# Kernel tuning notes

Measured on AMD Instinct MI355X. Metric: run time of the kernel, lower is better.

Reference implementation:

```python
import jax, jax.numpy as jnp
import numpy as np

EPS = 1e-6  # matches F.normalize / safe_div eps in vector-quantize-pytorch
IN_COMMIT_W = 0.25
COMMIT_W = 1.0


def _safe_div(num, den):
    return num / jnp.clip(den, EPS, None)


def _l2norm(t):
    n = jnp.linalg.norm(t, axis=-1, keepdims=True)
    return t / jnp.clip(n, EPS, None)


def setup_inputs() -> dict:
    key = jax.random.key(0)
    k1, k2, k3 = jax.random.split(key, 3)
    b, n, dim, c = 8, 1024, 512, 4096
    x = jax.random.normal(k1, (b, n, dim), jnp.float32)
    # frozen codebook init: randn * dim**-0.5 (as in __init__)
    frozen_codebook = jax.random.normal(k2, (c, dim), jnp.float32) * dim ** -0.5
    # nn.Linear(dim, dim, bias=False) weight, shape [out, in]
    weight = jax.random.normal(k3, (dim, dim), jnp.float32) * dim ** -0.5
    return {"x": x, "frozen_codebook": frozen_codebook, "weight": weight}


def simvq_forward(x, frozen_codebook, weight):
    # implicit codebook: frozen codes passed through linear transform -> [c, d]
    codebook = frozen_codebook @ weight.T

    # nearest-code search (torch.no_grad): squared distances have same argmin as cdist
    xs = jax.lax.stop_gradient(x)
    cs = jax.lax.stop_gradient(codebook)
    d2 = (jnp.sum(xs * xs, axis=-1, keepdims=True)
          - 2.0 * jnp.einsum('bnd,cd->bnc', xs, cs)
          + jnp.sum(cs * cs, axis=-1))  # [b, n, c]
    indices = jnp.argmin(d2, axis=-1)  # [b, n]

    quantized = codebook[indices]  # [b, n, d]

    # commitment loss: mse(x.detach(), q) + mse(x, q.detach()) * 0.25
    commit_loss = (jnp.mean((jax.lax.stop_gradient(x) - quantized) ** 2)
                   + IN_COMMIT_W * jnp.mean((x - jax.lax.stop_gradient(quantized)) ** 2))

    # rotation trick (Fifty et al.): rotate x onto quantized, grads flow as rotation
    nx = jnp.linalg.norm(x, axis=-1, keepdims=True)
    nq = jnp.linalg.norm(quantized, axis=-1, keepdims=True)
    u = _safe_div(x, nx)
    q = _safe_div(quantized, nq)
    w = jax.lax.stop_gradient(_l2norm(u + q))
    e = x
    ew = jnp.sum(e * w, axis=-1, keepdims=True)
    eu = jnp.sum(e * jax.lax.stop_gradient(u), axis=-1, keepdims=True)
    rotated = e - 2.0 * ew * w + 2.0 * eu * jax.lax.stop_gradient(q)
    rotated = rotated * jax.lax.stop_gradient(_safe_div(nq, nx))

    return rotated, indices, commit_loss * COMMIT_W


def reference(x, frozen_codebook, weight):
    return simvq_forward(x, frozen_codebook, weight)
```

## Files before the change

kernel.cpp:

```cpp
#include <hip/hip_runtime.h>
#include <hip/hip_bf16.h>
#include <cstdint>


#define R_ROWS 8192
#define DIM    512
#define NCODES 4096
#define BK     16
#define MARGIN      1.5e-2f
#define TILE_MARGIN 1.8e-2f

typedef __attribute__((ext_vector_type(8))) _Float16 f16x8;
typedef __attribute__((ext_vector_type(4))) float f32x4;
typedef __attribute__((ext_vector_type(8))) unsigned short ushort8;

__device__ __forceinline__ void gload_lds16(const void* g, void* l) {
    __builtin_amdgcn_global_load_lds(
        (const __attribute__((address_space(1))) void*)g,
        (__attribute__((address_space(3))) void*)l, 16, 0, 0);
}

template<int BM, int BN, int TM, int TN, bool ARGMIN>
__launch_bounds__(256)
__global__ void gemm_nt(const float* __restrict__ A, const float* __restrict__ Bm,
                        float* __restrict__ Cout,
                        const float* __restrict__ rowAdd, const float* __restrict__ colAdd,
                        float* __restrict__ pVal, int* __restrict__ pIdx,
                        int M, int N, int K) {
    constexpr int THREADS = (BM / TM) * (BN / TN);
    constexpr int PAD = 4;
    __shared__ float As[BK][BM + PAD];
    __shared__ float Bs[BK][BN + PAD];

    const int tid = threadIdx.x;
    const int tx = tid % (BN / TN);
    const int ty = tid / (BN / TN);
    const int rowBase = blockIdx.y * BM;
    const int colBase = blockIdx.x * BN;

    float acc[TM][TN];
#pragma unroll
    for (int i = 0; i < TM; i++)
#pragma unroll
        for (int j = 0; j < TN; j++) acc[i][j] = 0.f;

    constexpr int A_F4 = BM * BK / 4;
    constexpr int B_F4 = BN * BK / 4;
    const int nK = K / BK;

    for (int kt = 0; kt < nK; ++kt) {
        const int k0 = kt * BK;
#pragma unroll
        for (int f = 0; f < A_F4 / THREADS; ++f) {
            int e = tid + f * THREADS;
            int row = e >> 2;
            int kq = e & 3;
            float4 v = *reinterpret_cast<const float4*>(
                &A[(size_t)(rowBase + row) * K + k0 + kq * 4]);
            As[kq * 4 + 0][row] = v.x; As[kq * 4 + 1][row] = v.y;
            As[kq * 4 + 2][row] = v.z; As[kq * 4 + 3][row] = v.w;
        }
#pragma unroll
        for (int f = 0; f < B_F4 / THREADS; ++f) {
            int e = tid + f * THREADS;
            int row = e >> 2;
            int kq = e & 3;
            float4 v = *reinterpret_cast<const float4*>(
                &Bm[(size_t)(colBase + row) * K + k0 + kq * 4]);
            Bs[kq * 4 + 0][row] = v.x; Bs[kq * 4 + 1][row] = v.y;
            Bs[kq * 4 + 2][row] = v.z; Bs[kq * 4 + 3][row] = v.w;
        }
        __syncthreads();

#pragma unroll
        for (int k = 0; k < BK; k++) {
            float a[TM], b[TN];
#pragma unroll
            for (int i4 = 0; i4 < TM / 4; i4++) {
                float4 v = *reinterpret_cast<const float4*>(&As[k][ty * TM + i4 * 4]);
                a[i4 * 4 + 0] = v.x; a[i4 * 4 + 1] = v.y;
                a[i4 * 4 + 2] = v.z; a[i4 * 4 + 3] = v.w;
            }
#pragma unroll
            for (int j4 = 0; j4 < TN / 4; j4++) {
                float4 v = *reinterpret_cast<const float4*>(&Bs[k][tx * TN + j4 * 4]);
                b[j4 * 4 + 0] = v.x; b[j4 * 4 + 1] = v.y;
                b[j4 * 4 + 2] = v.z; b[j4 * 4 + 3] = v.w;
            }
#pragma unroll
            for (int i = 0; i < TM; i++)
#pragma unroll
                for (int j = 0; j < TN; j++) acc[i][j] = fmaf(a[i], b[j], acc[i][j]);
        }
        __syncthreads();
    }

    if constexpr (!ARGMIN) {
#pragma unroll
        for (int i = 0; i < TM; i++) {
#pragma unroll
            for (int j4 = 0; j4 < TN / 4; j4++) {
                float4 v = make_float4(acc[i][j4 * 4 + 0], acc[i][j4 * 4 + 1],
                                       acc[i][j4 * 4 + 2], acc[i][j4 * 4 + 3]);
                *reinterpret_cast<float4*>(
                    &Cout[(size_t)(rowBase + ty * TM + i) * N + colBase + tx * TN + j4 * 4]) = v;
            }
        }
    } else {
        constexpr int TX = BN / TN;
        __shared__ float rV[BM][TX + 1];
        __shared__ int   rI[BM][TX + 1];
        float xn[TM];
#pragma unroll
        for (int i = 0; i < TM; i++) xn[i] = rowAdd[rowBase + ty * TM + i];
        float cn[TN];
#pragma unroll
        for (int j = 0; j < TN; j++) cn[j] = colAdd[colBase + tx * TN + j];

#pragma unroll
        for (int i = 0; i < TM; i++) {
            float bv = 3.402823466e38f; int bi = 0;
#pragma unroll
            for (int j = 0; j < TN; j++) {
                float s = xn[i] + cn[j] - 2.f * acc[i][j];
                if (s < bv) { bv = s; bi = colBase + tx * TN + j; }
            }
            rV[ty * TM + i][tx] = bv;
            rI[ty * TM + i][tx] = bi;
        }
        __syncthreads();
        if (tid < BM) {
            float bv = 3.402823466e38f; int bi = 0;
#pragma unroll
            for (int t = 0; t < TX; t++) {
                float v = rV[tid][t];
                if (v < bv) { bv = v; bi = rI[tid][t]; }
            }
            int gr = rowBase + tid;
            pVal[(size_t)gr * gridDim.x + blockIdx.x] = bv;
            pIdx[(size_t)gr * gridDim.x + blockIdx.x] = bi;
        }
    }
}

__global__ void rowsumsq_cast(const float* __restrict__ src, float* __restrict__ dst,
                              ushort* __restrict__ h16, int nRows) {
    int gw = (blockIdx.x * blockDim.x + threadIdx.x) >> 6;
    int lane = threadIdx.x & 63;
    if (gw >= nRows) return;
    const float4* s4 = reinterpret_cast<const float4*>(src + (size_t)gw * DIM);
    float4 a = s4[lane];
    float4 b = s4[lane + 64];
    float s = a.x * a.x + a.y * a.y + a.z * a.z + a.w * a.w
            + b.x * b.x + b.y * b.y + b.z * b.z + b.w * b.w;

    ushort ha[4], hb[4];
    {
        _Float16 t0 = (_Float16)a.x, t1 = (_Float16)a.y,
                 t2 = (_Float16)a.z, t3 = (_Float16)a.w;
        ha[0] = *reinterpret_cast<unsigned short*>(&t0);
        ha[1] = *reinterpret_cast<unsigned short*>(&t1);
        ha[2] = *reinterpret_cast<unsigned short*>(&t2);
        ha[3] = *reinterpret_cast<unsigned short*>(&t3);
        _Float16 u0 = (_Float16)b.x, u1 = (_Float16)b.y,
                 u2 = (_Float16)b.z, u3 = (_Float16)b.w;
        hb[0] = *reinterpret_cast<unsigned short*>(&u0);
        hb[1] = *reinterpret_cast<unsigned short*>(&u1);
        hb[2] = *reinterpret_cast<unsigned short*>(&u2);
        hb[3] = *reinterpret_cast<unsigned short*>(&u3);
    }
    ushort* rowp = h16 + (size_t)gw * DIM;
    *reinterpret_cast<uint2*>(rowp + lane * 4)       = *reinterpret_cast<uint2*>(ha);
    *reinterpret_cast<uint2*>(rowp + 256 + lane * 4) = *reinterpret_cast<uint2*>(hb);

#pragma unroll
    for (int o = 32; o; o >>= 1) s += __shfl_xor(s, o);
    if (lane == 0) dst[gw] = s;
}

__global__ void rowsumsq(const float* __restrict__ src, float* __restrict__ dst, int nRows) {
    int gw = (blockIdx.x * blockDim.x + threadIdx.x) >> 6;
    int lane = threadIdx.x & 63;
    if (gw >= nRows) return;
    const float4* s4 = reinterpret_cast<const float4*>(src + (size_t)gw * DIM);
    float4 a = s4[lane];
    float4 b = s4[lane + 64];
    float s = a.x * a.x + a.y * a.y + a.z * a.z + a.w * a.w
            + b.x * b.x + b.y * b.y + b.z * b.z + b.w * b.w;
#pragma unroll
    for (int o = 32; o; o >>= 1) s += __shfl_xor(s, o);
    if (lane == 0) dst[gw] = s;
}

__device__ __forceinline__ f16x8 read_frag(const char* half_base, int row, int g) {
    int gp = g ^ ((row >> 1) & 3);
    return *reinterpret_cast<const f16x8*>(half_base + row * 64 + gp * 16);
}

__device__ __forceinline__ void stage128(const ushort* __restrict__ src, int rowBase,
                                         int segElem, char* ldsBase, int tid) {
#pragma unroll
    for (int i = 0; i < 2; ++i) {
        int o = i * 4096 + tid * 16;
        int row = o >> 6;
        int gp  = (o >> 4) & 3;
        int g   = gp ^ ((row >> 1) & 3);
        const char* gsrc = (const char*)src + (size_t)(rowBase + row) * 1024
                         + (size_t)segElem * 2 + g * 16;
        gload_lds16(gsrc, ldsBase + i * 4096 + (tid >> 6) * 1024);
    }
}

__launch_bounds__(256)
__global__ void score_mfma4(const ushort* __restrict__ xh, const ushort* __restrict__ ch,
                            const float* __restrict__ xn2, const float* __restrict__ cn2,
                            float* __restrict__ pV1, float* __restrict__ pV2,
                            int* __restrict__ pI1) {
    __shared__ __align__(16) ushort As[4096];
    __shared__ __align__(16) ushort Bs[4096];

    int bid = blockIdx.x;
    int swz = (bid & 7) * 256 + (bid >> 3);
    int tileN = swz & 31;
    int tileM = swz >> 5;
    int rowBase = tileM * 128, colBase = tileN * 128;

    int tid = threadIdx.x, lane = tid & 63, w = tid >> 6;
    int wr = w >> 1, wc = w & 1;
    int g = lane >> 4, c15 = lane & 15;

    f32x4 acc[4][4];
#pragma unroll
    for (int m = 0; m < 4; m++)
#pragma unroll
        for (int n = 0; n < 4; n++) acc[m][n] = (f32x4){0.f, 0.f, 0.f, 0.f};

    for (int kk = 0; kk < 16; ++kk) {
        int se = kk * 32;
        stage128(xh, rowBase, se, (char*)As, tid);
        stage128(ch, colBase, se, (char*)Bs, tid);
        __syncthreads();

        f16x8 af[4], bf[4];
#pragma unroll
        for (int m = 0; m < 4; ++m)
            af[m] = read_frag((const char*)As, wr * 64 + m * 16 + c15, g);
#pragma unroll
        for (int n = 0; n < 4; ++n)
            bf[n] = read_frag((const char*)Bs, wc * 64 + n * 16 + c15, g);
#pragma unroll
        for (int m = 0; m < 4; ++m)
#pragma unroll
            for (int n = 0; n < 4; ++n)
                acc[m][n] = __builtin_amdgcn_mfma_f32_16x16x32_f16(
                    af[m], bf[n], acc[m][n], 0, 0, 0);
        __syncthreads();
    }

    float cnv[4];
#pragma unroll
    for (int n = 0; n < 4; ++n) cnv[n] = cn2[colBase + wc * 64 + n * 16 + c15];

    size_t gbase = (size_t)(tileN * 2 + wc) * R_ROWS + rowBase;
#pragma unroll
    for (int m = 0; m < 4; ++m) {
#pragma unroll
        for (int j = 0; j < 4; ++j) {
            int rl = wr * 64 + m * 16 + g * 4 + j;
            float xn = xn2[rowBase + rl];
            float v1 = 3.402823466e38f, v2 = 3.402823466e38f; int i1 = 0x7fffffff;
#pragma unroll
            for (int n = 0; n < 4; ++n) {
                float s = xn + cnv[n] - 2.f * acc[m][n][j];
                int ci = colBase + wc * 64 + n * 16 + c15;
                if (s < v1 || (s == v1 && ci < i1)) { v2 = v1; v1 = s; i1 = ci; }
                else if (s < v2) v2 = s;
            }
#pragma unroll
            for (int off = 1; off < 16; off <<= 1) {
                float ov1 = __shfl_xor(v1, off);
                int   oi1 = __shfl_xor(i1, off);
                float ov2 = __shfl_xor(v2, off);
                if (ov1 < v1 || (ov1 == v1 && oi1 < i1)) {
                    v2 = fminf(v1, ov2); v1 = ov1; i1 = oi1;
                } else {
                    v2 = fminf(v2, ov1);
                }
            }
            if (c15 == 0) {
                size_t o = gbase + rl;
                pV1[o] = v1; pV2[o] = v2; pI1[o] = i1;
            }
        }
    }
}

__global__ void combine_flag(const float* __restrict__ pV1, const float* __restrict__ pV2,
                             const int* __restrict__ pI1,
                             int* __restrict__ idx, float* __restrict__ idxF,
                             int* __restrict__ flag, float* __restrict__ vminOut) {
    int r = blockIdx.x * blockDim.x + threadIdx.x;
    if (r >= R_ROWS) return;
    float v1 = 3.402823466e38f, v2 = 3.402823466e38f; int i1 = 0x7fffffff;
    for (int t = 0; t < 64; ++t) {
        float a1 = pV1[(size_t)t * R_ROWS + r];
        float a2 = pV2[(size_t)t * R_ROWS + r];
        int   ai = pI1[(size_t)t * R_ROWS + r];
        if (a1 < v1 || (a1 == v1 && ai < i1)) { v2 = fminf(v1, a2); v1 = a1; i1 = ai; }
        else { v2 = fminf(v2, a1); }
    }
    idx[r] = i1;
    idxF[r] = (float)i1;
    vminOut[r] = v1;
    flag[r] = (v2 - v1 < MARGIN) ? 1 : 0;
}

__launch_bounds__(256)
__global__ void refine_rows(const float* __restrict__ x, const float* __restrict__ cb,
                            const float* __restrict__ xn2, const float* __restrict__ cn2,
                            const float* __restrict__ pV1, const float* __restrict__ vmin,
                            const int* __restrict__ flag,
                            int* __restrict__ idx, float* __restrict__ idxF) {
    int r = blockIdx.x;
    if (flag[r] == 0) return;

    __shared__ float xs[DIM];
    __shared__ float wv[4];
    __shared__ int   wi[4];
    __shared__ unsigned long long maskS;
    int tid = threadIdx.x, lane = tid & 63, w = tid >> 6;

    for (int i = tid; i < DIM; i += 256) xs[i] = x[(size_t)r * DIM + i];

    float thr = vmin[r] + TILE_MARGIN;
    if (tid < 64) {
        float gm = pV1[(size_t)tid * R_ROWS + r];
        unsigned long long b = __ballot(gm <= thr);
        if (tid == 0) maskS = b;
    }
    __syncthreads();

    float x0 = xs[lane * 4 + 0], x1 = xs[lane * 4 + 1];
    float x2 = xs[lane * 4 + 2], x3 = xs[lane * 4 + 3];
    float y0 = xs[256 + lane * 4 + 0], y1 = xs[256 + lane * 4 + 1];
    float y2 = xs[256 + lane * 4 + 2], y3 = xs[256 + lane * 4 + 3];

    float xn = xn2[r];
    float v1 = 3.402823466e38f; int i1 = 0x7fffffff;

    unsigned long long mask = maskS;
    while (mask) {
        int gq = __ffsll((long long)mask) - 1;
        mask &= mask - 1;
#pragma unroll
        for (int t = 0; t < 4; ++t) {
            int c0 = gq * 64 + w * 4 + t * 16;
            const float4* cr0 = reinterpret_cast<const float4*>(cb + (size_t)(c0 + 0) * DIM);
            const float4* cr1 = reinterpret_cast<const float4*>(cb + (size_t)(c0 + 1) * DIM);
            const float4* cr2 = reinterpret_cast<const float4*>(cb + (size_t)(c0 + 2) * DIM);
            const float4* cr3 = reinterpret_cast<const float4*>(cb + (size_t)(c0 + 3) * DIM);
            float4 a0 = cr0[lane], b0 = cr0[lane + 64];
            float4 a1 = cr1[lane], b1 = cr1[lane + 64];
            float4 a2 = cr2[lane], b2 = cr2[lane + 64];
            float4 a3 = cr3[lane], b3 = cr3[lane + 64];
            float d0 = fmaf(x0, a0.x, fmaf(x1, a0.y, fmaf(x2, a0.z, fmaf(x3, a0.w,
                       fmaf(y0, b0.x, fmaf(y1, b0.y, fmaf(y2, b0.z, y3 * b0.w)))))));
            float d1 = fmaf(x0, a1.x, fmaf(x1, a1.y, fmaf(x2, a1.z, fmaf(x3, a1.w,
                       fmaf(y0, b1.x, fmaf(y1, b1.y, fmaf(y2, b1.z, y3 * b1.w)))))));
            float d2 = fmaf(x0, a2.x, fmaf(x1, a2.y, fmaf(x2, a2.z, fmaf(x3, a2.w,
                       fmaf(y0, b2.x, fmaf(y1, b2.y, fmaf(y2, b2.z, y3 * b2.w)))))));
            float d3 = fmaf(x0, a3.x, fmaf(x1, a3.y, fmaf(x2, a3.z, fmaf(x3, a3.w,
                       fmaf(y0, b3.x, fmaf(y1, b3.y, fmaf(y2, b3.z, y3 * b3.w)))))));
#pragma unroll
            for (int o = 32; o; o >>= 1) {
                d0 += __shfl_xor(d0, o);
                d1 += __shfl_xor(d1, o);
                d2 += __shfl_xor(d2, o);
                d3 += __shfl_xor(d3, o);
            }
            float s0 = xn + cn2[c0 + 0] - 2.f * d0;
            float s1 = xn + cn2[c0 + 1] - 2.f * d1;
            float s2 = xn + cn2[c0 + 2] - 2.f * d2;
            float s3 = xn + cn2[c0 + 3] - 2.f * d3;
            if (s0 < v1 || (s0 == v1 && (c0 + 0) < i1)) { v1 = s0; i1 = c0 + 0; }
            if (s1 < v1 || (s1 == v1 && (c0 + 1) < i1)) { v1 = s1; i1 = c0 + 1; }
            if (s2 < v1 || (s2 == v1 && (c0 + 2) < i1)) { v1 = s2; i1 = c0 + 2; }
            if (s3 < v1 || (s3 == v1 && (c0 + 3) < i1)) { v1 = s3; i1 = c0 + 3; }
        }
    }
    if (lane == 0) { wv[w] = v1; wi[w] = i1; }
    __syncthreads();
    if (tid == 0) {
        float bv = wv[0]; int bi = wi[0];
#pragma unroll
        for (int k = 1; k < 4; ++k) {
            if (wv[k] < bv || (wv[k] == bv && wi[k] < bi)) { bv = wv[k]; bi = wi[k]; }
        }
        idx[r] = bi; idxF[r] = (float)bi;
    }
}

__global__ void argmin_combine(const float* __restrict__ pVal, const int* __restrict__ pIdx,
                               int* __restrict__ idxOut, float* __restrict__ idxFloatOut,
                               int nTiles) {
    int r = blockIdx.x * blockDim.x + threadIdx.x;
    if (r >= R_ROWS) return;
    float bv = 3.402823466e38f; int bi = 0;
    for (int t = 0; t < nTiles; t++) {
        float v = pVal[(size_t)r * nTiles + t];
        if (v < bv) { bv = v; bi = pIdx[(size_t)r * nTiles + t]; }
    }
    idxOut[r] = bi;
    idxFloatOut[r] = (float)bi;
}

__global__ void rotate_rows(const float* __restrict__ x, const float* __restrict__ cb,
                            const int* __restrict__ idx, float* __restrict__ out,
                            float* __restrict__ lossPartial) {
    int gw = (blockIdx.x * blockDim.x + threadIdx.x) >> 6;
    int lane = threadIdx.x & 63;
    if (gw >= R_ROWS) return;

    const float4* x4 = reinterpret_cast<const float4*>(x + (size_t)gw * DIM);
    float4 xa = x4[lane], xb = x4[lane + 64];
    int ci = idx[gw];
    const float4* q4 = reinterpret_cast<const float4*>(cb + (size_t)ci * DIM);
    float4 qa = q4[lane], qb = q4[lane + 64];

    float xe[8] = {xa.x, xa.y, xa.z, xa.w, xb.x, xb.y, xb.z, xb.w};
    float qe[8] = {qa.x, qa.y, qa.z, qa.w, qb.x, qb.y, qb.z, qb.w};

    auto wsum = [&](float v) {
#pragma unroll
        for (int o = 32; o; o >>= 1) v += __shfl_xor(v, o);
        return v;
    };

    float lx = 0.f, lq = 0.f, ld = 0.f;
#pragma unroll
    for (int e = 0; e < 8; e++) {
        lx += xe[e] * xe[e];
        lq += qe[e] * qe[e];
        float d = xe[e] - qe[e];
        ld += d * d;
    }
    float sx2 = wsum(lx);
    float sq2 = wsum(lq);
    float lp  = wsum(ld);

    float nx = sqrtf(sx2), nq = sqrtf(sq2);
    float inx = 1.f / fmaxf(nx, 1e-6f);
    float inq = 1.f / fmaxf(nq, 1e-6f);

    float ue[8], qh[8], we[8];
    float lw = 0.f;
#pragma unroll
    for (int e = 0; e < 8; e++) {
        ue[e] = xe[e] * inx;
        qh[e] = qe[e] * inq;
        we[e] = ue[e] + qh[e];
        lw += we[e] * we[e];
    }
    float sw2 = wsum(lw);
    float inw = 1.f / fmaxf(sqrtf(sw2), 1e-6f);

    float lew = 0.f, leu = 0.f;
#pragma unroll
    for (int e = 0; e < 8; e++) {
        we[e] *= inw;
        lew += xe[e] * we[e];
        leu += xe[e] * ue[e];
    }
    float ew = wsum(lew);
    float eu = wsum(leu);

    float scale = nq / fmaxf(nx, 1e-6f);
    float oe[8];
#pragma unroll
    for (int e = 0; e < 8; e++)
        oe[e] = (xe[e] - 2.f * ew * we[e] + 2.f * eu * qh[e]) * scale;

    float4* o4 = reinterpret_cast<float4*>(out + (size_t)gw * DIM);
    o4[lane]      = make_float4(oe[0], oe[1], oe[2], oe[3]);
    o4[lane + 64] = make_float4(oe[4], oe[5], oe[6], oe[7]);

    if (lane == 0) lossPartial[gw] = lp;
}

__global__ void loss_reduce(const float* __restrict__ lp, float* __restrict__ outScalar) {
    __shared__ float red[256];
    float s = 0.f;
    for (int i = threadIdx.x; i < R_ROWS; i += 256) s += lp[i];
    red[threadIdx.x] = s;
    __syncthreads();
    for (int o = 128; o; o >>= 1) {
        if (threadIdx.x < o) red[threadIdx.x] += red[threadIdx.x + o];
        __syncthreads();
    }
    if (threadIdx.x == 0)
        outScalar[0] = 1.25f * red[0] / (float)(R_ROWS * DIM);
}

extern "C" void kernel_launch(void* const* d_in, const int* in_sizes, int n_in,
                              void* d_out, int out_size, void* d_ws, size_t ws_size,
                              hipStream_t stream) {
    const float* x      = (const float*)d_in[0];
    const float* frozen = (const float*)d_in[1];
    const float* weight = (const float*)d_in[2];
    float* out = (float*)d_out;

    char* p = (char*)d_ws;
    float* cb  = (float*)p;            p += (size_t)NCODES * DIM * 4;
    ushort* xh = (ushort*)p;           p += (size_t)R_ROWS * DIM * 2;
    ushort* ch = (ushort*)p;           p += (size_t)NCODES * DIM * 2;
    float* cn2 = (float*)p;            p += NCODES * 4;
    float* xn2 = (float*)p;            p += R_ROWS * 4;
    float* pV1 = (float*)p;            p += (size_t)R_ROWS * 64 * 4;
    float* pV2 = (float*)p;            p += (size_t)R_ROWS * 64 * 4;
    int*   pI1 = (int*)p;              p += (size_t)R_ROWS * 64 * 4;
    int*   idx = (int*)p;              p += R_ROWS * 4;
    int*   flg = (int*)p;              p += R_ROWS * 4;
    float* vmn = (float*)p;            p += R_ROWS * 4;
    float* lp  = (float*)p;            p += R_ROWS * 4;
    size_t need = (size_t)(p - (char*)d_ws);

    if (ws_size >= need) {
        dim3 g1(DIM / 64, NCODES / 64);
        gemm_nt<64, 64, 4, 4, false><<<g1, 256, 0, stream>>>(
            frozen, weight, cb, nullptr, nullptr, nullptr, nullptr, NCODES, DIM, DIM);

        rowsumsq_cast<<<R_ROWS / 4, 256, 0, stream>>>(x, xn2, xh, R_ROWS);
        rowsumsq_cast<<<NCODES / 4, 256, 0, stream>>>(cb, cn2, ch, NCODES);

        score_mfma4<<<(R_ROWS / 128) * (NCODES / 128), 256, 0, stream>>>(
            xh, ch, xn2, cn2, pV1, pV2, pI1);

        combine_flag<<<R_ROWS / 256, 256, 0, stream>>>(
            pV1, pV2, pI1, idx, out + (size_t)R_ROWS * DIM, flg, vmn);

        refine_rows<<<R_ROWS, 256, 0, stream>>>(
            x, cb, xn2, cn2, pV1, vmn, flg, idx, out + (size_t)R_ROWS * DIM);

        rotate_rows<<<R_ROWS / 4, 256, 0, stream>>>(x, cb, idx, out, lp);
        loss_reduce<<<1, 256, 0, stream>>>(lp, out + ((size_t)R_ROWS * DIM + R_ROWS));
    } else {
        float* fcn2 = (float*)((char*)d_ws + (size_t)NCODES * DIM * 4);
        float* fxn2 = fcn2 + NCODES;
        float* fpV = fxn2 + R_ROWS;
        int*   fpI = (int*)(fpV + (size_t)R_ROWS * 32);
        int*   fidx = (int*)(fpI + (size_t)R_ROWS * 32);
        float* flp = (float*)(fidx + R_ROWS);
        dim3 g1(DIM / 64, NCODES / 64);
        gemm_nt<64, 64, 4, 4, false><<<g1, 256, 0, stream>>>(
            frozen, weight, cb, nullptr, nullptr, nullptr, nullptr, NCODES, DIM, DIM);
        rowsumsq<<<NCODES / 4, 256, 0, stream>>>(cb, fcn2, NCODES);
        rowsumsq<<<R_ROWS / 4, 256, 0, stream>>>(x, fxn2, R_ROWS);
        dim3 g2(NCODES / 128, R_ROWS / 128);
        gemm_nt<128, 128, 8, 8, true><<<g2, 256, 0, stream>>>(
            x, cb, nullptr, fxn2, fcn2, fpV, fpI, R_ROWS, NCODES, DIM);
        argmin_combine<<<R_ROWS / 256, 256, 0, stream>>>(
            fpV, fpI, fidx, out + (size_t)R_ROWS * DIM, NCODES / 128);
        rotate_rows<<<R_ROWS / 4, 256, 0, stream>>>(x, cb, fidx, out, flp);
        loss_reduce<<<1, 256, 0, stream>>>(flp, out + ((size_t)R_ROWS * DIM + R_ROWS));
    }
}
```

Before: 195.9 us.

## Fuse partial-argmin combine, refinement and rotation into one per-row kernel

Merges three kernels into a single finalize_rows kernel with one block per row: combine_flag (merging the 64 tile partial minima), refine_rows (fp32 rescoring of ambiguous rows) and rotate_rows (rotation trick plus loss partial). The partial minima are now merged with wave shuffles, and the x row already staged in shared memory is reused for the rotation math. This removes two kernel launches and the global round trips for idx, flag and vmin. The trade-off is that rotation now runs with one wave per 256-thread block across 8192 blocks, so three of the four waves sit idle in that phase, which may lower efficiency compared with the old rotate kernel.

```diff
diff --git a/kernel.cpp b/kernel.cpp
--- a/kernel.cpp
+++ b/kernel.cpp
@@ -295,48 +295,43 @@
     }
 }
 
-__global__ void combine_flag(const float* __restrict__ pV1, const float* __restrict__ pV2,
-                             const int* __restrict__ pI1,
-                             int* __restrict__ idx, float* __restrict__ idxF,
-                             int* __restrict__ flag, float* __restrict__ vminOut) {
-    int r = blockIdx.x * blockDim.x + threadIdx.x;
-    if (r >= R_ROWS) return;
-    float v1 = 3.402823466e38f, v2 = 3.402823466e38f; int i1 = 0x7fffffff;
-    for (int t = 0; t < 64; ++t) {
-        float a1 = pV1[(size_t)t * R_ROWS + r];
-        float a2 = pV2[(size_t)t * R_ROWS + r];
-        int   ai = pI1[(size_t)t * R_ROWS + r];
-        if (a1 < v1 || (a1 == v1 && ai < i1)) { v2 = fminf(v1, a2); v1 = a1; i1 = ai; }
-        else { v2 = fminf(v2, a1); }
-    }
-    idx[r] = i1;
-    idxF[r] = (float)i1;
-    vminOut[r] = v1;
-    flag[r] = (v2 - v1 < MARGIN) ? 1 : 0;
-}
-
 __launch_bounds__(256)
-__global__ void refine_rows(const float* __restrict__ x, const float* __restrict__ cb,
-                            const float* __restrict__ xn2, const float* __restrict__ cn2,
-                            const float* __restrict__ pV1, const float* __restrict__ vmin,
-                            const int* __restrict__ flag,
-                            int* __restrict__ idx, float* __restrict__ idxF) {
+__global__ void finalize_rows(const float* __restrict__ x, const float* __restrict__ cb,
+                              const float* __restrict__ xn2, const float* __restrict__ cn2,
+                              const float* __restrict__ pV1, const float* __restrict__ pV2,
+                              const int* __restrict__ pI1,
+                              float* __restrict__ out, float* __restrict__ idxF,
+                              float* __restrict__ lossPartial) {
     int r = blockIdx.x;
-    if (flag[r] == 0) return;
+    int tid = threadIdx.x, lane = tid & 63, w = tid >> 6;
 
     __shared__ float xs[DIM];
     __shared__ float wv[4];
     __shared__ int   wi[4];
     __shared__ unsigned long long maskS;
-    int tid = threadIdx.x, lane = tid & 63, w = tid >> 6;
+    __shared__ int   idxS, flagS;
+    __shared__ float vminS;
 
     for (int i = tid; i < DIM; i += 256) xs[i] = x[(size_t)r * DIM + i];
 
-    float thr = vmin[r] + TILE_MARGIN;
-    if (tid < 64) {
-        float gm = pV1[(size_t)tid * R_ROWS + r];
-        unsigned long long b = __ballot(gm <= thr);
-        if (tid == 0) maskS = b;
+    if (w == 0) {
+        float a1 = pV1[(size_t)lane * R_ROWS + r];
+        float a2 = pV2[(size_t)lane * R_ROWS + r];
+        int   ai = pI1[(size_t)lane * R_ROWS + r];
+        float v1 = a1, v2 = a2; int i1 = ai;
+#pragma unroll
+        for (int off = 1; off < 64; off <<= 1) {
+            float o1 = __shfl_xor(v1, off);
+            float o2 = __shfl_xor(v2, off);
+            int   oi = __shfl_xor(i1, off);
+            if (o1 < v1 || (o1 == v1 && oi < i1)) { v2 = fminf(o2, v1); v1 = o1; i1 = oi; }
+            else { v2 = fminf(v2, o1); }
+        }
+        unsigned long long b = __ballot(a1 <= v1 + TILE_MARGIN);
+        if (lane == 0) {
+            maskS = b; idxS = i1; vminS = v1;
+            flagS = (v2 - v1 < MARGIN) ? 1 : 0;
+        }
     }
     __syncthreads();
 
@@ -344,59 +339,129 @@
     float x2 = xs[lane * 4 + 2], x3 = xs[lane * 4 + 3];
     float y0 = xs[256 + lane * 4 + 0], y1 = xs[256 + lane * 4 + 1];
     float y2 = xs[256 + lane * 4 + 2], y3 = xs[256 + lane * 4 + 3];
-
     float xn = xn2[r];
-    float v1 = 3.402823466e38f; int i1 = 0x7fffffff;
-
-    unsigned long long mask = maskS;
-    while (mask) {
-        int gq = __ffsll((long long)mask) - 1;
-        mask &= mask - 1;
-#pragma unroll
-        for (int t = 0; t < 4; ++t) {
-            int c0 = gq * 64 + w * 4 + t * 16;
-            const float4* cr0 = reinterpret_cast<const float4*>(cb + (size_t)(c0 + 0) * DIM);
-            const float4* cr1 = reinterpret_cast<const float4*>(cb + (size_t)(c0 + 1) * DIM);
-            const float4* cr2 = reinterpret_cast<const float4*>(cb + (size_t)(c0 + 2) * DIM);
-            const float4* cr3 = reinterpret_cast<const float4*>(cb + (size_t)(c0 + 3) * DIM);
-            float4 a0 = cr0[lane], b0 = cr0[lane + 64];
-            float4 a1 = cr1[lane], b1 = cr1[lane + 64];
-            float4 a2 = cr2[lane], b2 = cr2[lane + 64];
-            float4 a3 = cr3[lane], b3 = cr3[lane + 64];
-            float d0 = fmaf(x0, a0.x, fmaf(x1, a0.y, fmaf(x2, a0.z, fmaf(x3, a0.w,
-                       fmaf(y0, b0.x, fmaf(y1, b0.y, fmaf(y2, b0.z, y3 * b0.w)))))));
-            float d1 = fmaf(x0, a1.x, fmaf(x1, a1.y, fmaf(x2, a1.z, fmaf(x3, a1.w,
-                       fmaf(y0, b1.x, fmaf(y1, b1.y, fmaf(y2, b1.z, y3 * b1.w)))))));
-            float d2 = fmaf(x0, a2.x, fmaf(x1, a2.y, fmaf(x2, a2.z, fmaf(x3, a2.w,
-                       fmaf(y0, b2.x, fmaf(y1, b2.y, fmaf(y2, b2.z, y3 * b2.w)))))));
-            float d3 = fmaf(x0, a3.x, fmaf(x1, a3.y, fmaf(x2, a3.z, fmaf(x3, a3.w,
-                       fmaf(y0, b3.x, fmaf(y1, b3.y, fmaf(y2, b3.z, y3 * b3.w)))))));
-#pragma unroll
-            for (int o = 32; o; o >>= 1) {
-                d0 += __shfl_xor(d0, o);
-                d1 += __shfl_xor(d1, o);
-                d2 += __shfl_xor(d2, o);
-                d3 += __shfl_xor(d3, o);
-            }
-            float s0 = xn + cn2[c0 + 0] - 2.f * d0;
-            float s1 = xn + cn2[c0 + 1] - 2.f * d1;
-            float s2 = xn + cn2[c0 + 2] - 2.f * d2;
-            float s3 = xn + cn2[c0 + 3] - 2.f * d3;
-            if (s0 < v1 || (s0 == v1 && (c0 + 0) < i1)) { v1 = s0; i1 = c0 + 0; }
-            if (s1 < v1 || (s1 == v1 && (c0 + 1) < i1)) { v1 = s1; i1 = c0 + 1; }
-            if (s2 < v1 || (s2 == v1 && (c0 + 2) < i1)) { v1 = s2; i1 = c0 + 2; }
-            if (s3 < v1 || (s3 == v1 && (c0 + 3) < i1)) { v1 = s3; i1 = c0 + 3; }
-        }
-    }
-    if (lane == 0) { wv[w] = v1; wi[w] = i1; }
-    __syncthreads();
-    if (tid == 0) {
-        float bv = wv[0]; int bi = wi[0];
-#pragma unroll
-        for (int k = 1; k < 4; ++k) {
-            if (wv[k] < bv || (wv[k] == bv && wi[k] < bi)) { bv = wv[k]; bi = wi[k]; }
-        }
-        idx[r] = bi; idxF[r] = (float)bi;
+
+    if (flagS) {
+        float v1 = 3.402823466e38f; int i1 = 0x7fffffff;
+        unsigned long long mask = maskS;
+        while (mask) {
+            int gq = __ffsll((long long)mask) - 1;
+            mask &= mask - 1;
+#pragma unroll
+            for (int t = 0; t < 4; ++t) {
+                int c0 = gq * 64 + w * 4 + t * 16;
+                const float4* cr0 = reinterpret_cast<const float4*>(cb + (size_t)(c0 + 0) * DIM);
+                const float4* cr1 = reinterpret_cast<const float4*>(cb + (size_t)(c0 + 1) * DIM);
+                const float4* cr2 = reinterpret_cast<const float4*>(cb + (size_t)(c0 + 2) * DIM);
+                const float4* cr3 = reinterpret_cast<const float4*>(cb + (size_t)(c0 + 3) * DIM);
+                float4 a0 = cr0[lane], b0 = cr0[lane + 64];
+                float4 a1 = cr1[lane], b1 = cr1[lane + 64];
+                float4 a2 = cr2[lane], b2 = cr2[lane + 64];
+                float4 a3 = cr3[lane], b3 = cr3[lane + 64];
+                float d0 = fmaf(x0, a0.x, fmaf(x1, a0.y, fmaf(x2, a0.z, fmaf(x3, a0.w,
+                           fmaf(y0, b0.x, fmaf(y1, b0.y, fmaf(y2, b0.z, y3 * b0.w)))))));
+                float d1 = fmaf(x0, a1.x, fmaf(x1, a1.y, fmaf(x2, a1.z, fmaf(x3, a1.w,
+                           fmaf(y0, b1.x, fmaf(y1, b1.y, fmaf(y2, b1.z, y3 * b1.w)))))));
+                float d2 = fmaf(x0, a2.x, fmaf(x1, a2.y, fmaf(x2, a2.z, fmaf(x3, a2.w,
+                           fmaf(y0, b2.x, fmaf(y1, b2.y, fmaf(y2, b2.z, y3 * b2.w)))))));
+                float d3 = fmaf(x0, a3.x, fmaf(x1, a3.y, fmaf(x2, a3.z, fmaf(x3, a3.w,
+                           fmaf(y0, b3.x, fmaf(y1, b3.y, fmaf(y2, b3.z, y3 * b3.w)))))));
+#pragma unroll
+                for (int o = 32; o; o >>= 1) {
+                    d0 += __shfl_xor(d0, o);
+                    d1 += __shfl_xor(d1, o);
+                    d2 += __shfl_xor(d2, o);
+                    d3 += __shfl_xor(d3, o);
+                }
+                float s0 = xn + cn2[c0 + 0] - 2.f * d0;
+                float s1 = xn + cn2[c0 + 1] - 2.f * d1;
+                float s2 = xn + cn2[c0 + 2] - 2.f * d2;
+                float s3 = xn + cn2[c0 + 3] - 2.f * d3;
+                if (s0 < v1 || (s0 == v1 && (c0 + 0) < i1)) { v1 = s0; i1 = c0 + 0; }
+                if (s1 < v1 || (s1 == v1 && (c0 + 1) < i1)) { v1 = s1; i1 = c0 + 1; }
+                if (s2 < v1 || (s2 == v1 && (c0 + 2) < i1)) { v1 = s2; i1 = c0 + 2; }
+                if (s3 < v1 || (s3 == v1 && (c0 + 3) < i1)) { v1 = s3; i1 = c0 + 3; }
+            }
+        }
+        if (lane == 0) { wv[w] = v1; wi[w] = i1; }
+        __syncthreads();
+        if (tid == 0) {
+            float bv = wv[0]; int bi = wi[0];
+#pragma unroll
+            for (int k = 1; k < 4; ++k) {
+                if (wv[k] < bv || (wv[k] == bv && wi[k] < bi)) { bv = wv[k]; bi = wi[k]; }
+            }
+            idxS = bi;
+        }
+        __syncthreads();
+    }
+
+    if (w == 0) {
+        int ci = idxS;
+        const float4* q4 = reinterpret_cast<const float4*>(cb + (size_t)ci * DIM);
+        float4 qa = q4[lane], qb = q4[lane + 64];
+
+        float xe[8] = {x0, x1, x2, x3, y0, y1, y2, y3};
+        float qe[8] = {qa.x, qa.y, qa.z, qa.w, qb.x, qb.y, qb.z, qb.w};
+
+        auto wsum = [&](float v) {
+#pragma unroll
+            for (int o = 32; o; o >>= 1) v += __shfl_xor(v, o);
+            return v;
+        };
+
+        float lx = 0.f, lq = 0.f, ld = 0.f;
+#pragma unroll
+        for (int e = 0; e < 8; e++) {
+            lx += xe[e] * xe[e];
+            lq += qe[e] * qe[e];
+            float d = xe[e] - qe[e];
+            ld += d * d;
+        }
+        float sx2 = wsum(lx);
+        float sq2 = wsum(lq);
+        float lp  = wsum(ld);
+
+        float nx = sqrtf(sx2), nq = sqrtf(sq2);
+        float inx = 1.f / fmaxf(nx, 1e-6f);
+        float inq = 1.f / fmaxf(nq, 1e-6f);
+
+        float ue[8], qh[8], we[8];
+        float lw = 0.f;
+#pragma unroll
+        for (int e = 0; e < 8; e++) {
+            ue[e] = xe[e] * inx;
+            qh[e] = qe[e] * inq;
+            we[e] = ue[e] + qh[e];
+            lw += we[e] * we[e];
+        }
+        float sw2 = wsum(lw);
+        float inw = 1.f / fmaxf(sqrtf(sw2), 1e-6f);
+
+        float lew = 0.f, leu = 0.f;
+#pragma unroll
+        for (int e = 0; e < 8; e++) {
+            we[e] *= inw;
+            lew += xe[e] * we[e];
+            leu += xe[e] * ue[e];
+        }
+        float ew = wsum(lew);
+        float eu = wsum(leu);
+
+        float scale = nq / fmaxf(nx, 1e-6f);
+        float oe[8];
+#pragma unroll
+        for (int e = 0; e < 8; e++)
+            oe[e] = (xe[e] - 2.f * ew * we[e] + 2.f * eu * qh[e]) * scale;
+
+        float4* o4 = reinterpret_cast<float4*>(out + (size_t)r * DIM);
+        o4[lane]      = make_float4(oe[0], oe[1], oe[2], oe[3]);
+        o4[lane + 64] = make_float4(oe[4], oe[5], oe[6], oe[7]);
+
+        if (lane == 0) {
+            lossPartial[r] = lp;
+            idxF[r] = (float)idxS;
+        }
     }
 }
 
@@ -535,13 +600,10 @@
         score_mfma4<<<(R_ROWS / 128) * (NCODES / 128), 256, 0, stream>>>(
             xh, ch, xn2, cn2, pV1, pV2, pI1);
 
-        combine_flag<<<R_ROWS / 256, 256, 0, stream>>>(
-            pV1, pV2, pI1, idx, out + (size_t)R_ROWS * DIM, flg, vmn);
-
-        refine_rows<<<R_ROWS, 256, 0, stream>>>(
-            x, cb, xn2, cn2, pV1, vmn, flg, idx, out + (size_t)R_ROWS * DIM);
-
-        rotate_rows<<<R_ROWS / 4, 256, 0, stream>>>(x, cb, idx, out, lp);
+        finalize_rows<<<R_ROWS, 256, 0, stream>>>(
+            x, cb, xn2, cn2, pV1, pV2, pI1,
+            out, out + (size_t)R_ROWS * DIM, lp);
+
         loss_reduce<<<1, 256, 0, stream>>>(lp, out + ((size_t)R_ROWS * DIM + R_ROWS));
     } else {
         float* fcn2 = (float*)((char*)d_ws + (size_t)NCODES * DIM * 4);
```

Result: faster. 164.5 us (-16.0%).
